# Optimization experiments

Hardware: AMD Instinct MI355X
Metric: run time of the kernel (lower is better)

## Reference

```python
import jax, jax.numpy as jnp
import numpy as np

L, N, D, B_, T = 4, 4, 2048, 2, 2048  # num_blocks, expansion_rate, dim, batch, seq


def setup_inputs() -> dict:
    key = jax.random.key(0)
    ks = jax.random.split(key, 12)
    f = lambda k, sh, s=0.02: s * jax.random.normal(k, sh, jnp.float32)
    x = jax.random.normal(ks[0], (B_, T, D), jnp.float32)
    # structural torch inits + small noise so grads/kernels are exercised
    eyecols = jnp.stack([jnp.eye(N, dtype=jnp.float32)[:, [i % N]] for i in range(L)])  # [L,N,1]
    A_m = eyecols + f(ks[1], (L, N, 1), 0.05)
    A_r = jnp.broadcast_to(jnp.eye(N, dtype=jnp.float32), (L, N, N)) + f(ks[2], (L, N, N), 0.05)
    Bp = jnp.ones((L, 1, N), jnp.float32) + f(ks[3], (L, 1, N), 0.05)
    W_m = f(ks[4], (L, D, 1))
    W_r = f(ks[5], (L, D, N))
    W_b = f(ks[6], (L, D, N))
    s_a = 0.01 * jnp.ones((L, 1, 1), jnp.float32)
    s_b = 0.01 * jnp.ones((L, 1, 1), jnp.float32)
    dyn_gamma = jnp.ones((L, D), jnp.float32) + f(ks[7], (L, D), 0.05)   # LayerNorm(bias=False)
    norm_gamma = jnp.ones((L, D), jnp.float32) + f(ks[8], (L, D), 0.05)  # per-block norm weight
    norm_beta = f(ks[9], (L, D))                                          # per-block norm bias
    Wblk = f(ks[10], (L, D, D), 1.0) / np.sqrt(D)                         # block = Linear(D, D)
    bblk = f(ks[11], (L, D))
    return dict(x=x, A_m=A_m, A_r=A_r, Bp=Bp, W_m=W_m, W_r=W_r, W_b=W_b,
                s_a=s_a, s_b=s_b, dyn_gamma=dyn_gamma, norm_gamma=norm_gamma,
                norm_beta=norm_beta, Wblk=Wblk, bblk=bblk)


def _ln(x, gamma, beta=None, eps=1e-5):
    mu = jnp.mean(x, axis=-1, keepdims=True)
    var = jnp.mean(jnp.square(x - mu), axis=-1, keepdims=True)
    y = (x - mu) * jax.lax.rsqrt(var + eps) * gamma
    return y if beta is None else y + beta


def reference(x, A_m, A_r, Bp, W_m, W_r, W_b, s_a, s_b,
              dyn_gamma, norm_gamma, norm_beta, Wblk, bblk):
    # hyper branch (n > 0), dynamic=True, pre_norm=True
    H = jnp.repeat(x[:, :, None, :], N, axis=2)  # [B,T,N,D]
    for i in range(L):
        # ---- width connections ----
        Hn = _ln(H, dyn_gamma[i])                                              # dynamic LN, no bias
        Am = A_m[i] + s_a[i] * jnp.tanh(jnp.einsum('btnd,do->btno', Hn, W_m[i]))  # [B,T,N,1]
        Ar = A_r[i] + s_a[i] * jnp.tanh(jnp.einsum('btnd,dm->btnm', Hn, W_r[i]))  # [B,T,N,N]
        WC = jnp.concatenate([Am, Ar], axis=-1)                                # [B,T,N,1+N]
        Ht = jnp.einsum('btnd,btnm->btdm', H, WC)                              # H^T @ WC
        h = Ht[..., 0]                                                         # [B,T,D]
        H = jnp.swapaxes(Ht[..., 1:], -2, -1)                                  # [B,T,N,D]
        # ---- pre-norm + block ----
        h = _ln(h, norm_gamma[i], norm_beta[i])
        h = jnp.einsum('btd,de->bte', h, Wblk[i]) + bblk[i]
        # ---- depth connections ----
        hn = _ln(h, dyn_gamma[i])
        Bv = Bp[i][0] + s_b[i] * jnp.tanh(jnp.einsum('btd,dn->btn', hn, W_b[i]))  # [B,T,N]
        H = H + h[:, :, None, :] * Bv[..., None]
    return H.sum(axis=2)  # [B,T,D]
```

## Files before the change

kernel.cpp:

```cpp
#include <hip/hip_runtime.h>
#include <hip/hip_bf16.h>


#define DD 2048
#define NN 4
#define LL 4
#define NTOK 4096
#define EPSF 1e-5f

typedef __attribute__((ext_vector_type(8))) short bf16x8;
typedef __attribute__((ext_vector_type(4))) float f32x4;
typedef __attribute__((ext_vector_type(2))) float f32x2;

__device__ __forceinline__ float bf2f(short u) {
  union { unsigned int i; float f; } v;
  v.i = ((unsigned int)(unsigned short)u) << 16;
  return v.f;
}
__device__ __forceinline__ short f2bf(float f) {
  __hip_bfloat16 h = __float2bfloat16(f);
  short s;
  __builtin_memcpy(&s, &h, 2);
  return s;
}
__device__ __forceinline__ float wred(float v) {
#pragma unroll
  for (int off = 32; off > 0; off >>= 1) v += __shfl_xor(v, off, 64);
  return v;
}
__device__ __forceinline__ void ld16(const void* g, void* l) {
  __builtin_amdgcn_global_load_lds(
      (const __attribute__((address_space(1))) void*)g,
      (__attribute__((address_space(3))) void*)l, 16, 0, 0);
}

__global__ __launch_bounds__(256) void prep_pack(
    const float* __restrict__ W_m, const float* __restrict__ W_r,
    const float* __restrict__ W_b, const float* __restrict__ dyn_gamma,
    const float* __restrict__ norm_gamma, const float* __restrict__ norm_beta,
    short* __restrict__ gwm, short* __restrict__ gwr, short* __restrict__ gwb,
    float* __restrict__ rb) {
  const int i = blockIdx.x * 256 + threadIdx.x;
  const float g = dyn_gamma[i];
  gwm[i] = f2bf(g * W_m[i]);
  f32x4 r = *(const f32x4*)(W_r + (size_t)i * 4);
  f32x4 b = *(const f32x4*)(W_b + (size_t)i * 4);
  short ro[4], bo[4];
#pragma unroll
  for (int k = 0; k < 4; k++) { ro[k] = f2bf(g * r[k]); bo[k] = f2bf(g * b[k]); }
  *(unsigned long long*)(gwr + (size_t)i * 4) = *(unsigned long long*)ro;
  *(unsigned long long*)(gwb + (size_t)i * 4) = *(unsigned long long*)bo;
  rb[i] = norm_beta[i] / norm_gamma[i];
}

__global__ __launch_bounds__(64) void prep_sums(
    const float* __restrict__ W_m, const float* __restrict__ W_r,
    const float* __restrict__ W_b, const float* __restrict__ dyn_gamma,
    float* __restrict__ S0w, float* __restrict__ T0d) {
  const int l = blockIdx.x;
  const int lane = threadIdx.x;
  float s[5] = {0, 0, 0, 0, 0}, t[4] = {0, 0, 0, 0};
  for (int d = lane; d < DD; d += 64) {
    const float g = dyn_gamma[l * DD + d];
    s[0] += g * W_m[l * DD + d];
    f32x4 r = *(const f32x4*)(W_r + ((size_t)l * DD + d) * 4);
    f32x4 b = *(const f32x4*)(W_b + ((size_t)l * DD + d) * 4);
#pragma unroll
    for (int m = 0; m < 4; m++) { s[1 + m] += g * r[m]; t[m] += g * b[m]; }
  }
#pragma unroll
  for (int m = 0; m < 5; m++) s[m] = wred(s[m]);
#pragma unroll
  for (int n = 0; n < 4; n++) t[n] = wred(t[n]);
  if (lane == 0) {
#pragma unroll
    for (int m = 0; m < 5; m++) S0w[l * 5 + m] = s[m];
#pragma unroll
    for (int n = 0; n < 4; n++) T0d[l * 4 + n] = t[n];
  }
}

__global__ __launch_bounds__(256) void transpose_wblk(
    const float* __restrict__ W, const float* __restrict__ norm_gamma,
    short* __restrict__ Wt) {
  __shared__ float tile[64][65];
  const int blk = blockIdx.z;
  const int c0 = blockIdx.x * 64;
  const int r0 = blockIdx.y * 64;
  const float* Ws = W + (size_t)blk * DD * DD;
  short* Wd = Wt + (size_t)blk * DD * DD;
  const int tx = threadIdx.x & 63, ty = threadIdx.x >> 6;
#pragma unroll
  for (int r = 0; r < 16; r++) {
    const int row = ty + r * 4;
    tile[row][tx] = Ws[(size_t)(r0 + row) * DD + c0 + tx];
  }
  const float gsc = norm_gamma[blk * DD + r0 + tx];
  __syncthreads();
#pragma unroll
  for (int r = 0; r < 16; r++) {
    const int row = ty + r * 4;
    Wd[(size_t)(c0 + row) * DD + r0 + tx] = f2bf(tile[tx][row] * gsc);
  }
}

__global__ __launch_bounds__(256) void row_sums(
    const short* __restrict__ Wt, const float* __restrict__ rb,
    const float* __restrict__ bblk, float* __restrict__ E0,
    float* __restrict__ E1) {
  const int l = blockIdx.y;
  const int e = blockIdx.x * 4 + (threadIdx.x >> 6);
  const int lane = threadIdx.x & 63;
  const short* row = Wt + ((size_t)l * DD + e) * DD;
  const float* rbl = rb + l * DD;
  float s1 = 0.f, s0 = 0.f;
#pragma unroll
  for (int it = 0; it < 4; it++) {
    const int d0 = lane * 8 + it * 512;
    bf16x8 w = *(const bf16x8*)(row + d0);
    f32x4 r0 = *(const f32x4*)(rbl + d0), r1 = *(const f32x4*)(rbl + d0 + 4);
#pragma unroll
    for (int q = 0; q < 8; q++) {
      const float wq = bf2f(w[q]);
      s1 += wq;
      s0 += wq * ((q < 4) ? r0[q] : r1[q - 4]);
    }
  }
  s1 = wred(s1); s0 = wred(s0);
  if (lane == 0) {
    E1[l * DD + e] = s1;
    E0[l * DD + e] = s0 + bblk[l * DD + e];
  }
}

__global__ __launch_bounds__(256) void width0_kernel(
    const float* __restrict__ x, short* __restrict__ Hst,
    short* __restrict__ hout, f32x2* __restrict__ tst,
    const float* __restrict__ A_m, const float* __restrict__ A_r,
    const short* __restrict__ gwm, const short* __restrict__ gwr,
    const float* __restrict__ s_a, const float* __restrict__ S0w) {
  const int wave = threadIdx.x >> 6;
  const int lane = threadIdx.x & 63;
  const int tok = blockIdx.x * 4 + wave;
  const int blk = 0;
  const short* wm = gwm + blk * DD;
  const short* wr = gwr + (size_t)blk * DD * 4;

  bf16x8 hreg[4];
  const float* xr = x + (size_t)tok * DD;
#pragma unroll
  for (int j = 0; j < 4; j++) {
    const int d0 = lane * 8 + j * 512;
    f32x4 a = *(const f32x4*)(xr + d0);
    f32x4 b = *(const f32x4*)(xr + d0 + 4);
    bf16x8 p;
#pragma unroll
    for (int q = 0; q < 4; q++) { p[q] = f2bf(a[q]); p[4 + q] = f2bf(b[q]); }
    hreg[j] = p;
  }

  float sH = 0, sH2 = 0, S1[5] = {0, 0, 0, 0, 0};
#pragma unroll
  for (int j = 0; j < 4; j++) {
    const int d0 = lane * 8 + j * 512;
    bf16x8 mv = *(const bf16x8*)(wm + d0);
    bf16x8 wv[4];
#pragma unroll
    for (int p = 0; p < 4; p++)
      wv[p] = *(const bf16x8*)(wr + (size_t)(d0 + 2 * p) * 4);
#pragma unroll
    for (int q = 0; q < 8; q++) {
      const float hv = bf2f(hreg[j][q]);
      sH += hv; sH2 += hv * hv;
      S1[0] += hv * bf2f(mv[q]);
#pragma unroll
      for (int m = 0; m < 4; m++)
        S1[1 + m] += hv * bf2f(wv[q >> 1][(q & 1) * 4 + m]);
    }
  }
  sH = wred(sH); sH2 = wred(sH2);
#pragma unroll
  for (int m = 0; m < 5; m++) S1[m] = wred(S1[m]);

  const float sa = s_a[blk];
  const float mu0 = sH * (1.f / DD);
  const float inv0 = rsqrtf(sH2 * (1.f / DD) - mu0 * mu0 + EPSF);
  float amSum = 0.f, arCol[NN] = {0, 0, 0, 0};
  {
    const float t0 = tanhf(inv0 * (S1[0] - mu0 * S0w[blk * 5 + 0]));
    float tm[NN];
#pragma unroll
    for (int m = 0; m < NN; m++)
      tm[m] = tanhf(inv0 * (S1[1 + m] - mu0 * S0w[blk * 5 + 1 + m]));
#pragma unroll
    for (int n = 0; n < NN; n++) {
      amSum += A_m[blk * NN + n] + sa * t0;
#pragma unroll
      for (int m = 0; m < NN; m++)
        arCol[m] += A_r[blk * NN * NN + n * NN + m] + sa * tm[m];
    }
  }

  short* Ho = Hst + (size_t)tok * NN * DD;
  short* hw = hout + (size_t)tok * DD;
  float sh = 0.f, sh2 = 0.f;
#pragma unroll
  for (int j = 0; j < 4; j++) {
    const int d0 = lane * 8 + j * 512;
    bf16x8 outp[NN], ho;
#pragma unroll
    for (int q = 0; q < 8; q++) {
      const float hv = bf2f(hreg[j][q]);
      const float a0 = hv * amSum;
      sh += a0; sh2 += a0 * a0;
      ho[q] = f2bf(a0);
#pragma unroll
      for (int m = 0; m < NN; m++) outp[m][q] = f2bf(hv * arCol[m]);
    }
    *(bf16x8*)(hw + d0) = ho;
#pragma unroll
    for (int m = 0; m < NN; m++) *(bf16x8*)(Ho + m * DD + d0) = outp[m];
  }
  sh = wred(sh); sh2 = wred(sh2);
  if (lane == 0) {
    const float mu = sh * (1.f / DD);
    const float inv = rsqrtf(sh2 * (1.f / DD) - mu * mu + EPSF);
    f32x2 t; t[0] = inv; t[1] = mu * inv;
    tst[tok] = t;
  }
}

__global__ __launch_bounds__(256) void gemm_kernel(
    const short* __restrict__ A, const short* __restrict__ Bt,
    const f32x2* __restrict__ tst, const float* __restrict__ E0,
    const float* __restrict__ E1, short* __restrict__ C) {
  __shared__ short lA[2][128 * 64];
  __shared__ short lB[2][128 * 64];
  const int tid = threadIdx.x;
  const int lane = tid & 63;
  const int wave = tid >> 6;
  const int m0 = blockIdx.x * 128, n0 = blockIdx.y * 128;
  const int wm = wave >> 1, wn = wave & 1;

  f32x4 acc[4][4] = {};

#define STAGE(buf, kt)                                                        \
  {                                                                           \
    const int k0 = (kt) * 64;                                                 \
    _Pragma("unroll") for (int c = 0; c < 4; c++) {                           \
      const int idx = c * 256 + tid;                                          \
      const int row = idx >> 3;                                               \
      const int colsw = (((idx & 7) ^ (row & 7)) * 8);                        \
      ld16(A + (size_t)(m0 + row) * DD + k0 + colsw,                          \
           (char*)&lA[buf][0] + idx * 16);                                    \
      ld16(Bt + (size_t)(n0 + row) * DD + k0 + colsw,                         \
           (char*)&lB[buf][0] + idx * 16);                                    \
    }                                                                         \
  }

  STAGE(0, 0);
  __syncthreads();

  for (int kt = 0; kt < 32; ++kt) {
    const int cur = kt & 1;
    if (kt < 31) STAGE(cur ^ 1, kt + 1);
    const char* bufA = (const char*)&lA[cur][0];
    const char* bufB = (const char*)&lB[cur][0];
#pragma unroll
    for (int kk = 0; kk < 2; ++kk) {
      const int gsw = (kk * 64 + (lane >> 4) * 16) ^ ((lane & 7) << 4);
      bf16x8 af[4], bfr[4];
#pragma unroll
      for (int m = 0; m < 4; m++) {
        const int r = wm * 64 + m * 16 + (lane & 15);
        af[m] = *(const bf16x8*)(bufA + r * 128 + gsw);
      }
#pragma unroll
      for (int n = 0; n < 4; n++) {
        const int r = wn * 64 + n * 16 + (lane & 15);
        bfr[n] = *(const bf16x8*)(bufB + r * 128 + gsw);
      }
#pragma unroll
      for (int m = 0; m < 4; m++)
#pragma unroll
        for (int n = 0; n < 4; n++)
          acc[m][n] = __builtin_amdgcn_mfma_f32_16x16x32_bf16(
              af[m], bfr[n], acc[m][n], 0, 0, 0);
    }
    __syncthreads();
  }
#undef STAGE

  float e0c[4], e1c[4];
  int cols[4];
#pragma unroll
  for (int n = 0; n < 4; n++) {
    cols[n] = n0 + wn * 64 + n * 16 + (lane & 15);
    e0c[n] = E0[cols[n]];
    e1c[n] = E1[cols[n]];
  }
#pragma unroll
  for (int m = 0; m < 4; m++) {
    const int rbase = m0 + wm * 64 + m * 16 + ((lane >> 4) << 2);
#pragma unroll
    for (int j = 0; j < 4; j++) {
      const int row = rbase + j;
      const f32x2 iv = tst[row];
#pragma unroll
      for (int n = 0; n < 4; n++)
        C[(size_t)row * DD + cols[n]] =
            f2bf(iv[0] * acc[m][n][j] - iv[1] * e1c[n] + e0c[n]);
    }
  }
}

__global__ __launch_bounds__(256) void fused_dw(
    const short* __restrict__ h2, short* __restrict__ Hst,
    short* __restrict__ hout, f32x2* __restrict__ tst,
    const float* __restrict__ Bp, const short* __restrict__ gwb,
    const float* __restrict__ s_b, const float* __restrict__ A_m,
    const float* __restrict__ A_r, const short* __restrict__ gwm,
    const short* __restrict__ gwr, const float* __restrict__ s_a,
    const float* __restrict__ S0w, const float* __restrict__ T0d, int blk) {
  const int wave = threadIdx.x >> 6;
  const int lane = threadIdx.x & 63;
  const int tok = blockIdx.x * 4 + wave;
  const int nblk = blk + 1;
  const short* hr = h2 + (size_t)tok * DD;
  short* Ho = Hst + (size_t)tok * NN * DD;

  bf16x8 h2r[4], hold[NN][4];
#pragma unroll
  for (int j = 0; j < 4; j++) {
    const int d0 = lane * 8 + j * 512;
    h2r[j] = *(const bf16x8*)(hr + d0);
#pragma unroll
    for (int n = 0; n < NN; n++)
      hold[n][j] = *(const bf16x8*)(Ho + n * DD + d0);
  }

  const short* wb = gwb + (size_t)blk * DD * 4;
  float s1 = 0.f, s2 = 0.f, T1[NN] = {0, 0, 0, 0};
#pragma unroll
  for (int j = 0; j < 4; j++) {
    const int d0 = lane * 8 + j * 512;
    bf16x8 wv[4];
#pragma unroll
    for (int p = 0; p < 4; p++)
      wv[p] = *(const bf16x8*)(wb + (size_t)(d0 + 2 * p) * 4);
#pragma unroll
    for (int q = 0; q < 8; q++) {
      const float hv = bf2f(h2r[j][q]);
      s1 += hv; s2 += hv * hv;
#pragma unroll
      for (int n = 0; n < NN; n++)
        T1[n] += hv * bf2f(wv[q >> 1][(q & 1) * 4 + n]);
    }
  }
  s1 = wred(s1); s2 = wred(s2);
#pragma unroll
  for (int n = 0; n < NN; n++) T1[n] = wred(T1[n]);
  float Bv[NN];
  {
    const float mu = s1 * (1.f / DD);
    const float inv = rsqrtf(s2 * (1.f / DD) - mu * mu + EPSF);
    const float sb = s_b[blk];
#pragma unroll
    for (int n = 0; n < NN; n++)
      Bv[n] = Bp[blk * NN + n] +
              sb * tanhf(inv * (T1[n] - mu * T0d[blk * NN + n]));
  }
#pragma unroll
  for (int n = 0; n < NN; n++)
#pragma unroll
    for (int j = 0; j < 4; j++) {
      bf16x8 o;
#pragma unroll
      for (int q = 0; q < 8; q++)
        o[q] = f2bf(bf2f(hold[n][j][q]) + bf2f(h2r[j][q]) * Bv[n]);
      hold[n][j] = o;
    }

  const short* wm = gwm + nblk * DD;
  const short* wr = gwr + (size_t)nblk * DD * 4;
  float sH[NN] = {0, 0, 0, 0}, sH2[NN] = {0, 0, 0, 0};
  float S1[NN][5];
#pragma unroll
  for (int n = 0; n < NN; n++)
#pragma unroll
    for (int m = 0; m < 5; m++) S1[n][m] = 0.f;

#pragma unroll
  for (int j = 0; j < 4; j++) {
    const int d0 = lane * 8 + j * 512;
    bf16x8 mv = *(const bf16x8*)(wm + d0);
    bf16x8 wv[4];
#pragma unroll
    for (int p = 0; p < 4; p++)
      wv[p] = *(const bf16x8*)(wr + (size_t)(d0 + 2 * p) * 4);
#pragma unroll
    for (int q = 0; q < 8; q++) {
      float gw[5];
      gw[0] = bf2f(mv[q]);
#pragma unroll
      for (int m = 0; m < 4; m++)
        gw[1 + m] = bf2f(wv[q >> 1][(q & 1) * 4 + m]);
#pragma unroll
      for (int n = 0; n < NN; n++) {
        const float hv = bf2f(hold[n][j][q]);
        sH[n] += hv; sH2[n] += hv * hv;
#pragma unroll
        for (int m = 0; m < 5; m++) S1[n][m] += hv * gw[m];
      }
    }
  }
#pragma unroll
  for (int n = 0; n < NN; n++) { sH[n] = wred(sH[n]); sH2[n] = wred(sH2[n]); }
#pragma unroll
  for (int n = 0; n < NN; n++)
#pragma unroll
    for (int m = 0; m < 5; m++) S1[n][m] = wred(S1[n][m]);

  const float sa = s_a[nblk];
  float Am[NN], Ar[NN][NN];
#pragma unroll
  for (int n = 0; n < NN; n++) {
    const float mu = sH[n] * (1.f / DD);
    const float var = sH2[n] * (1.f / DD) - mu * mu;
    const float inv = rsqrtf(var + EPSF);
    Am[n] = A_m[nblk * NN + n] +
            sa * tanhf(inv * (S1[n][0] - mu * S0w[nblk * 5 + 0]));
#pragma unroll
    for (int m = 0; m < NN; m++)
      Ar[n][m] = A_r[nblk * NN * NN + n * NN + m] +
                 sa * tanhf(inv * (S1[n][1 + m] - mu * S0w[nblk * 5 + 1 + m]));
  }

  short* hw = hout + (size_t)tok * DD;
  float sh = 0.f, sh2 = 0.f;
#pragma unroll
  for (int j = 0; j < 4; j++) {
    const int d0 = lane * 8 + j * 512;
    bf16x8 outp[NN], ho;
#pragma unroll
    for (int q = 0; q < 8; q++) {
      float a0 = 0.f, am0 = 0.f, am1 = 0.f, am2 = 0.f, am3 = 0.f;
#pragma unroll
      for (int n = 0; n < NN; n++) {
        const float hv = bf2f(hold[n][j][q]);
        a0 += hv * Am[n];
        am0 += hv * Ar[n][0];
        am1 += hv * Ar[n][1];
        am2 += hv * Ar[n][2];
        am3 += hv * Ar[n][3];
      }
      sh += a0; sh2 += a0 * a0;
      ho[q] = f2bf(a0);
      outp[0][q] = f2bf(am0); outp[1][q] = f2bf(am1);
      outp[2][q] = f2bf(am2); outp[3][q] = f2bf(am3);
    }
    *(bf16x8*)(hw + d0) = ho;
#pragma unroll
    for (int m = 0; m < NN; m++) *(bf16x8*)(Ho + m * DD + d0) = outp[m];
  }
  sh = wred(sh); sh2 = wred(sh2);
  if (lane == 0) {
    const float mu = sh * (1.f / DD);
    const float inv = rsqrtf(sh2 * (1.f / DD) - mu * mu + EPSF);
    f32x2 t; t[0] = inv; t[1] = mu * inv;
    tst[tok] = t;
  }
}

__global__ __launch_bounds__(256) void depth_last(
    const short* __restrict__ h2, const short* __restrict__ Hst,
    float* __restrict__ out, const float* __restrict__ Bp,
    const short* __restrict__ gwb, const float* __restrict__ s_b,
    const float* __restrict__ T0d, int blk) {
  const int wave = threadIdx.x >> 6;
  const int lane = threadIdx.x & 63;
  const int tok = blockIdx.x * 4 + wave;
  const short* hr = h2 + (size_t)tok * DD;
  const short* wb = gwb + (size_t)blk * DD * 4;

  bf16x8 h2r[4];
  float s1 = 0.f, s2 = 0.f, T1[NN] = {0, 0, 0, 0};
#pragma unroll
  for (int j = 0; j < 4; j++) {
    const int d0 = lane * 8 + j * 512;
    h2r[j] = *(const bf16x8*)(hr + d0);
    bf16x8 wv[4];
#pragma unroll
    for (int p = 0; p < 4; p++)
      wv[p] = *(const bf16x8*)(wb + (size_t)(d0 + 2 * p) * 4);
#pragma unroll
    for (int q = 0; q < 8; q++) {
      const float hv = bf2f(h2r[j][q]);
      s1 += hv; s2 += hv * hv;
#pragma unroll
      for (int n = 0; n < NN; n++)
        T1[n] += hv * bf2f(wv[q >> 1][(q & 1) * 4 + n]);
    }
  }
  s1 = wred(s1); s2 = wred(s2);
#pragma unroll
  for (int n = 0; n < NN; n++) T1[n] = wred(T1[n]);
  const float mu = s1 * (1.f / DD);
  const float inv = rsqrtf(s2 * (1.f / DD) - mu * mu + EPSF);
  const float sb = s_b[blk];
  float bsum = 0.f;
#pragma unroll
  for (int n = 0; n < NN; n++)
    bsum += Bp[blk * NN + n] + sb * tanhf(inv * (T1[n] - mu * T0d[blk * NN + n]));

  const short* Ho = Hst + (size_t)tok * NN * DD;
  float* orow = out + (size_t)tok * DD;
#pragma unroll
  for (int j = 0; j < 4; j++) {
    const int d0 = lane * 8 + j * 512;
    bf16x8 hrow[NN];
#pragma unroll
    for (int n = 0; n < NN; n++) hrow[n] = *(const bf16x8*)(Ho + n * DD + d0);
    f32x4 o0, o1;
#pragma unroll
    for (int q = 0; q < 8; q++) {
      const float hv = bf2f(h2r[j][q]);
      float s = hv * bsum;
#pragma unroll
      for (int n = 0; n < NN; n++) s += bf2f(hrow[n][q]);
      if (q < 4) o0[q] = s; else o1[q - 4] = s;
    }
    *(f32x4*)(orow + d0) = o0;
    *(f32x4*)(orow + d0 + 4) = o1;
  }
}

extern "C" void kernel_launch(void* const* d_in, const int* in_sizes, int n_in,
                              void* d_out, int out_size, void* d_ws,
                              size_t ws_size, hipStream_t stream) {
  const float* x = (const float*)d_in[0];
  const float* A_m = (const float*)d_in[1];
  const float* A_r = (const float*)d_in[2];
  const float* Bp = (const float*)d_in[3];
  const float* W_m = (const float*)d_in[4];
  const float* W_r = (const float*)d_in[5];
  const float* W_b = (const float*)d_in[6];
  const float* s_a = (const float*)d_in[7];
  const float* s_b = (const float*)d_in[8];
  const float* dyn_gamma = (const float*)d_in[9];
  const float* norm_gamma = (const float*)d_in[10];
  const float* norm_beta = (const float*)d_in[11];
  const float* Wblk = (const float*)d_in[12];
  const float* bblk = (const float*)d_in[13];
  float* out = (float*)d_out;

  char* ws = (char*)d_ws;
  short* Hst = (short*)(ws);
  short* hbuf = (short*)(ws + 67108864);
  short* h2 = (short*)(ws + 83886080);
  char* aux = ws + 100663296;
  short* gwm = (short*)(aux);
  short* gwr = (short*)(aux + 16384);
  short* gwb = (short*)(aux + 16384 + 65536);
  float* rb = (float*)(aux + 16384 + 131072);
  float* S0w = (float*)(aux + 16384 + 131072 + 32768);
  float* T0d = (float*)(aux + 16384 + 131072 + 32768 + 128);
  f32x2* tst = (f32x2*)(aux + 16384 + 131072 + 32768 + 256);
  float* E0 = (float*)(aux + 16384 + 131072 + 32768 + 256 + 32768);
  float* E1 = E0 + LL * DD;
  short* Wt = (short*)d_out;

  dim3 tb(256);
  prep_pack<<<32, tb, 0, stream>>>(W_m, W_r, W_b, dyn_gamma, norm_gamma,
                                   norm_beta, gwm, gwr, gwb, rb);
  prep_sums<<<4, dim3(64), 0, stream>>>(W_m, W_r, W_b, dyn_gamma, S0w, T0d);
  transpose_wblk<<<dim3(32, 32, 4), tb, 0, stream>>>(Wblk, norm_gamma, Wt);
  row_sums<<<dim3(512, 4), tb, 0, stream>>>(Wt, rb, bblk, E0, E1);
  width0_kernel<<<1024, tb, 0, stream>>>(x, Hst, hbuf, tst, A_m, A_r, gwm,
                                         gwr, s_a, S0w);
  for (int i = 0; i < LL; i++) {
    gemm_kernel<<<dim3(32, 16), tb, 0, stream>>>(
        hbuf, Wt + (size_t)i * DD * DD, tst, E0 + i * DD, E1 + i * DD, h2);
    if (i < LL - 1)
      fused_dw<<<1024, tb, 0, stream>>>(h2, Hst, hbuf, tst, Bp, gwb, s_b, A_m,
                                        A_r, gwm, gwr, s_a, S0w, T0d, i);
    else
      depth_last<<<1024, tb, 0, stream>>>(h2, Hst, out, Bp, gwb, s_b, T0d, i);
  }
}
```

Measured before the change: 390.8 us.

## Use 8-wave GEMM with XCD-aware block remap; reload H in fused_dw

The GEMM now runs 512 threads per 128x128 tile, each of the 8 waves computing a 64x32 sub-tile, which halves accumulators per wave and doubles the waves available to hide latency. A 1D grid is remapped so consecutive blocks on the same XCD share tiles. fused_dw no longer keeps all 16 H vectors in registers; it reloads H from global memory in each pass and recomputes the depth update on the fly, lowering register pressure at the cost of an extra read of H. The recomputation also skips the intermediate bf16 rounding of the updated H.

```diff
diff --git a/kernel.cpp b/kernel.cpp
--- a/kernel.cpp
+++ b/kernel.cpp
@@ -230,7 +230,7 @@
   }
 }
 
-__global__ __launch_bounds__(256) void gemm_kernel(
+__global__ __launch_bounds__(512) void gemm_kernel(
     const short* __restrict__ A, const short* __restrict__ Bt,
     const f32x2* __restrict__ tst, const float* __restrict__ E0,
     const float* __restrict__ E1, short* __restrict__ C) {
@@ -239,16 +239,19 @@
   const int tid = threadIdx.x;
   const int lane = tid & 63;
   const int wave = tid >> 6;
-  const int m0 = blockIdx.x * 128, n0 = blockIdx.y * 128;
-  const int wm = wave >> 1, wn = wave & 1;
-
-  f32x4 acc[4][4] = {};
+  const int bid = blockIdx.x;
+  const int wg = (bid & 7) * 64 + (bid >> 3);
+  const int m0 = (wg & 31) * 128, n0 = (wg >> 5) * 128;
+  const int wm = wave >> 2;
+  const int wn = wave & 3;
+
+  f32x4 acc[4][2] = {};
 
 #define STAGE(buf, kt)                                                        \
   {                                                                           \
     const int k0 = (kt) * 64;                                                 \
-    _Pragma("unroll") for (int c = 0; c < 4; c++) {                           \
-      const int idx = c * 256 + tid;                                          \
+    _Pragma("unroll") for (int c = 0; c < 2; c++) {                           \
+      const int idx = c * 512 + tid;                                          \
       const int row = idx >> 3;                                               \
       const int colsw = (((idx & 7) ^ (row & 7)) * 8);                        \
       ld16(A + (size_t)(m0 + row) * DD + k0 + colsw,                          \
@@ -269,21 +272,21 @@
 #pragma unroll
     for (int kk = 0; kk < 2; ++kk) {
       const int gsw = (kk * 64 + (lane >> 4) * 16) ^ ((lane & 7) << 4);
-      bf16x8 af[4], bfr[4];
+      bf16x8 af[4], bfr[2];
 #pragma unroll
       for (int m = 0; m < 4; m++) {
         const int r = wm * 64 + m * 16 + (lane & 15);
         af[m] = *(const bf16x8*)(bufA + r * 128 + gsw);
       }
 #pragma unroll
-      for (int n = 0; n < 4; n++) {
-        const int r = wn * 64 + n * 16 + (lane & 15);
+      for (int n = 0; n < 2; n++) {
+        const int r = wn * 32 + n * 16 + (lane & 15);
         bfr[n] = *(const bf16x8*)(bufB + r * 128 + gsw);
       }
 #pragma unroll
       for (int m = 0; m < 4; m++)
 #pragma unroll
-        for (int n = 0; n < 4; n++)
+        for (int n = 0; n < 2; n++)
           acc[m][n] = __builtin_amdgcn_mfma_f32_16x16x32_bf16(
               af[m], bfr[n], acc[m][n], 0, 0, 0);
     }
@@ -291,11 +294,11 @@
   }
 #undef STAGE
 
-  float e0c[4], e1c[4];
-  int cols[4];
-#pragma unroll
-  for (int n = 0; n < 4; n++) {
-    cols[n] = n0 + wn * 64 + n * 16 + (lane & 15);
+  float e0c[2], e1c[2];
+  int cols[2];
+#pragma unroll
+  for (int n = 0; n < 2; n++) {
+    cols[n] = n0 + wn * 32 + n * 16 + (lane & 15);
     e0c[n] = E0[cols[n]];
     e1c[n] = E1[cols[n]];
   }
@@ -307,7 +310,7 @@
       const int row = rbase + j;
       const f32x2 iv = tst[row];
 #pragma unroll
-      for (int n = 0; n < 4; n++)
+      for (int n = 0; n < 2; n++)
         C[(size_t)row * DD + cols[n]] =
             f2bf(iv[0] * acc[m][n][j] - iv[1] * e1c[n] + e0c[n]);
     }
@@ -329,15 +332,10 @@
   const short* hr = h2 + (size_t)tok * DD;
   short* Ho = Hst + (size_t)tok * NN * DD;
 
-  bf16x8 h2r[4], hold[NN][4];
-#pragma unroll
-  for (int j = 0; j < 4; j++) {
-    const int d0 = lane * 8 + j * 512;
-    h2r[j] = *(const bf16x8*)(hr + d0);
-#pragma unroll
-    for (int n = 0; n < NN; n++)
-      hold[n][j] = *(const bf16x8*)(Ho + n * DD + d0);
-  }
+  bf16x8 h2r[4];
+#pragma unroll
+  for (int j = 0; j < 4; j++)
+    h2r[j] = *(const bf16x8*)(hr + lane * 8 + j * 512);
 
   const short* wb = gwb + (size_t)blk * DD * 4;
   float s1 = 0.f, s2 = 0.f, T1[NN] = {0, 0, 0, 0};
@@ -370,16 +368,6 @@
       Bv[n] = Bp[blk * NN + n] +
               sb * tanhf(inv * (T1[n] - mu * T0d[blk * NN + n]));
   }
-#pragma unroll
-  for (int n = 0; n < NN; n++)
-#pragma unroll
-    for (int j = 0; j < 4; j++) {
-      bf16x8 o;
-#pragma unroll
-      for (int q = 0; q < 8; q++)
-        o[q] = f2bf(bf2f(hold[n][j][q]) + bf2f(h2r[j][q]) * Bv[n]);
-      hold[n][j] = o;
-    }
 
   const short* wm = gwm + nblk * DD;
   const short* wr = gwr + (size_t)nblk * DD * 4;
@@ -393,6 +381,9 @@
 #pragma unroll
   for (int j = 0; j < 4; j++) {
     const int d0 = lane * 8 + j * 512;
+    bf16x8 hold[NN];
+#pragma unroll
+    for (int n = 0; n < NN; n++) hold[n] = *(const bf16x8*)(Ho + n * DD + d0);
     bf16x8 mv = *(const bf16x8*)(wm + d0);
     bf16x8 wv[4];
 #pragma unroll
@@ -400,6 +391,7 @@
       wv[p] = *(const bf16x8*)(wr + (size_t)(d0 + 2 * p) * 4);
 #pragma unroll
     for (int q = 0; q < 8; q++) {
+      const float hv2 = bf2f(h2r[j][q]);
       float gw[5];
       gw[0] = bf2f(mv[q]);
 #pragma unroll
@@ -407,10 +399,10 @@
         gw[1 + m] = bf2f(wv[q >> 1][(q & 1) * 4 + m]);
 #pragma unroll
       for (int n = 0; n < NN; n++) {
-        const float hv = bf2f(hold[n][j][q]);
-        sH[n] += hv; sH2[n] += hv * hv;
-#pragma unroll
-        for (int m = 0; m < 5; m++) S1[n][m] += hv * gw[m];
+        const float hp = bf2f(hold[n][q]) + hv2 * Bv[n];
+        sH[n] += hp; sH2[n] += hp * hp;
+#pragma unroll
+        for (int m = 0; m < 5; m++) S1[n][m] += hp * gw[m];
       }
     }
   }
@@ -441,18 +433,24 @@
 #pragma unroll
   for (int j = 0; j < 4; j++) {
     const int d0 = lane * 8 + j * 512;
+    bf16x8 hold[NN];
+#pragma unroll
+    for (int n = 0; n < NN; n++) hold[n] = *(const bf16x8*)(Ho + n * DD + d0);
     bf16x8 outp[NN], ho;
 #pragma unroll
     for (int q = 0; q < 8; q++) {
+      const float hv2 = bf2f(h2r[j][q]);
+      float hp[NN];
+#pragma unroll
+      for (int n = 0; n < NN; n++) hp[n] = bf2f(hold[n][q]) + hv2 * Bv[n];
       float a0 = 0.f, am0 = 0.f, am1 = 0.f, am2 = 0.f, am3 = 0.f;
 #pragma unroll
       for (int n = 0; n < NN; n++) {
-        const float hv = bf2f(hold[n][j][q]);
-        a0 += hv * Am[n];
-        am0 += hv * Ar[n][0];
-        am1 += hv * Ar[n][1];
-        am2 += hv * Ar[n][2];
-        am3 += hv * Ar[n][3];
+        a0 += hp[n] * Am[n];
+        am0 += hp[n] * Ar[n][0];
+        am1 += hp[n] * Ar[n][1];
+        am2 += hp[n] * Ar[n][2];
+        am3 += hp[n] * Ar[n][3];
       }
       sh += a0; sh2 += a0 * a0;
       ho[q] = f2bf(a0);
@@ -579,7 +577,7 @@
   width0_kernel<<<1024, tb, 0, stream>>>(x, Hst, hbuf, tst, A_m, A_r, gwm,
                                          gwr, s_a, S0w);
   for (int i = 0; i < LL; i++) {
-    gemm_kernel<<<dim3(32, 16), tb, 0, stream>>>(
+    gemm_kernel<<<512, dim3(512), 0, stream>>>(
         hbuf, Wt + (size_t)i * DD * DD, tst, E0 + i * DD, E1 + i * DD, h2);
     if (i < LL - 1)
       fused_dw<<<1024, tb, 0, stream>>>(h2, Hst, hbuf, tst, Bp, gwb, s_b, A_m,
```

Result: faster. 369.1 us (-5.5%).
